# Kernel tuning notes

Measured on AMD Instinct MI355X. Metric: run time of the kernel, lower is better.

Reference implementation:

```python
import jax, jax.numpy as jnp
import numpy as np

NUM_QUBITS = 12
DIM = 2 ** NUM_QUBITS  # 4096
BATCH = 2048
TWO_PI = 2.0 * np.pi


def _diag_phases(p0, p1):
    """Kronecker product of per-qubit diag(exp(i*p0[k]), exp(i*p1[k])) matrices,
    represented as the length-2^n diagonal vector. Phases add under kron of
    diagonal exponentials, so accumulate phases and exponentiate once."""
    ph = jnp.zeros((1,), jnp.float32)
    n = p0.shape[0]
    for k in range(n):  # loop over qubits (small, structural)
        ph = (ph[:, None] + jnp.stack([p0[k], p1[k]])[None, :]).reshape(-1)
    return jnp.exp(1j * ph)  # complex64 diagonal of the 2^n x 2^n operator


def _bs_matrix(n):
    """n-fold Kronecker product of the 50/50 beamsplitter matrix."""
    inv_sqrt2 = np.float32(1.0 / np.sqrt(2.0))
    bs = jnp.array([[1.0, 1j], [1j, 1.0]], dtype=jnp.complex64) * inv_sqrt2
    M = jnp.ones((1, 1), dtype=jnp.complex64)
    for _ in range(n):
        M = jnp.kron(M, bs)
    return M  # [2^n, 2^n]


def setup_inputs() -> dict:
    key = jax.random.key(0)
    k1, k2, k3, k4, k5, k6 = jax.random.split(key, 6)
    return {
        "x_real": jax.random.normal(k1, (BATCH, DIM), dtype=jnp.float32),
        "x_imag": jax.random.normal(k2, (BATCH, DIM), dtype=jnp.float32),
        "alphas": jax.random.uniform(k3, (NUM_QUBITS,), dtype=jnp.float32, maxval=TWO_PI),
        "betas": jax.random.uniform(k4, (NUM_QUBITS,), dtype=jnp.float32, maxval=TWO_PI),
        "thetas": jax.random.uniform(k5, (NUM_QUBITS,), dtype=jnp.float32, maxval=TWO_PI),
        "phis": jax.random.uniform(k6, (NUM_QUBITS,), dtype=jnp.float32, maxval=TWO_PI),
    }


def reference(x_real, x_imag, alphas, betas, thetas, phis):
    x = x_real + 1j * x_imag  # [B, 2^n] complex64
    zeros = jnp.zeros_like(thetas)
    d_in = _diag_phases(alphas, betas)   # input_shifts diagonal
    d_th = _diag_phases(thetas, zeros)   # theta_shifts diagonal
    d_ph = _diag_phases(phis, zeros)     # phi_shifts diagonal
    bs = _bs_matrix(NUM_QUBITS)          # dense tensor-product matrix
    # K.dot(x, M) == x @ M; diagonal matmuls become row-wise elementwise scales.
    out = (x * d_in) @ bs
    out = (out * d_th) @ bs
    out = out * d_ph
    return out
```

## Files before the change

### kernel.cpp

```cpp
#include <hip/hip_runtime.h>
#include <math.h>

#define NQ 12
#define DIM 4096
#define BATCH 2048

typedef float fv4 __attribute__((ext_vector_type(4)));
typedef float fv2 __attribute__((ext_vector_type(2)));

#if defined(__has_builtin)
#if __has_builtin(__builtin_nontemporal_load) && __has_builtin(__builtin_nontemporal_store)
#define NT_LOAD(p)     __builtin_nontemporal_load(p)
#define NT_STORE(p, v) __builtin_nontemporal_store((v), (p))
#endif
#endif
#ifndef NT_LOAD
#define NT_LOAD(p)     (*(p))
#define NT_STORE(p, v) (*(p) = (v))
#endif

__device__ __forceinline__ float2 cmulf(float2 a, float2 b) {
    return make_float2(a.x * b.x - a.y * b.y, a.x * b.y + a.y * b.x);
}

__device__ __forceinline__ void gstage(float (&vr)[16], float (&vi)[16],
                                       float2 m00, float2 m01,
                                       float2 m10, float2 m11, int m) {
#pragma unroll
    for (int r = 0; r < 16; ++r) {
        if (r & m) continue;
        const int p = r | m;
        const float ur = vr[r], ui = vi[r], wr = vr[p], wi = vi[p];
        vr[r] = fmaf(ur, m00.x, fmaf(-ui, m00.y, fmaf(wr, m10.x, -wi * m10.y)));
        vi[r] = fmaf(ur, m00.y, fmaf( ui, m00.x, fmaf(wr, m10.y,  wi * m10.x)));
        vr[p] = fmaf(ur, m01.x, fmaf(-ui, m01.y, fmaf(wr, m11.x, -wi * m11.y)));
        vi[p] = fmaf(ur, m01.y, fmaf( ui, m01.x, fmaf(wr, m11.y,  wi * m11.x)));
    }
}

__device__ __forceinline__ void apply4(float (&vr)[16], float (&vi)[16],
                                       const float2 (*mt)[4],
                                       int q1, int q2, int q4, int q8) {
    float2 a0 = mt[q1][0], a1 = mt[q1][1], a2 = mt[q1][2], a3 = mt[q1][3];
    float2 b0 = mt[q2][0], b1 = mt[q2][1], b2 = mt[q2][2], b3 = mt[q2][3];
    float2 c0 = mt[q4][0], c1 = mt[q4][1], c2 = mt[q4][2], c3 = mt[q4][3];
    float2 d0 = mt[q8][0], d1 = mt[q8][1], d2 = mt[q8][2], d3 = mt[q8][3];
    gstage(vr, vi, a0, a1, a2, a3, 1);
    gstage(vr, vi, b0, b1, b2, b3, 2);
    gstage(vr, vi, c0, c1, c2, c3, 4);
    gstage(vr, vi, d0, d1, d2, d3, 8);
}

template <bool INTERLEAVED>
__global__ __launch_bounds__(256, 4) void qlayer(
        const float* __restrict__ xr, const float* __restrict__ xi,
        const float* __restrict__ alphas, const float* __restrict__ betas,
        const float* __restrict__ thetas, const float* __restrict__ phis,
        float* __restrict__ out) {
    __shared__ float2 lds[DIM];
    __shared__ float2 mt[NQ][4];

    const int t = threadIdx.x;
    const int row = blockIdx.x;
    const int w = t >> 6, l = t & 63;
    const int abase = (w << 10) | (l << 4);

    fv4 lre[4], lim[4];
    {
        const float* xrp = xr + (size_t)row * DIM + abase;
        const float* xip = xi + (size_t)row * DIM + abase;
#pragma unroll
        for (int c = 0; c < 4; ++c) {
            lre[c] = NT_LOAD(reinterpret_cast<const fv4*>(xrp + 4 * c));
            lim[c] = NT_LOAD(reinterpret_cast<const fv4*>(xip + 4 * c));
        }
    }

    if (t < NQ) {
        float sa, ca;
        sincosf(thetas[t], &sa, &ca);
        const float2 h0 = make_float2((ca - 1.f) * 0.5f, sa * 0.5f);
        const float2 h1 = make_float2(-sa * 0.5f, (ca + 1.f) * 0.5f);
        const float al = alphas[t], be = betas[t], ph = phis[t];
        float s, c;
        sincosf(al + ph, &s, &c); mt[t][0] = cmulf(make_float2(c, s), h0);
        sincosf(al, &s, &c);      mt[t][1] = cmulf(make_float2(c, s), h1);
        sincosf(be + ph, &s, &c); mt[t][2] = cmulf(make_float2(c, s), h1);
        sincosf(be, &s, &c);      mt[t][3] = cmulf(make_float2(c, s),
                                                   make_float2(-h0.x, -h0.y));
    }
    __syncthreads();

    float vr[16], vi[16];
#pragma unroll
    for (int c = 0; c < 4; ++c)
#pragma unroll
        for (int j = 0; j < 4; ++j) {
            vr[c * 4 + j] = lre[c][j];
            vi[c * 4 + j] = lim[c][j];
        }

    apply4(vr, vi, mt, 11, 10, 9, 8);

    const int wbase = w << 10;
#pragma unroll
    for (int r = 0; r < 16; ++r) {
        const int s = wbase | (l << 4) | (r ^ (l & 15));
        lds[s] = make_float2(vr[r], vi[r]);
    }
    asm volatile("s_waitcnt lgkmcnt(0)" ::: "memory");
#pragma unroll
    for (int r = 0; r < 16; ++r) {
        const int s = wbase | ((l >> 4) << 8) | (r << 4) | ((l & 15) ^ r);
        const float2 v = lds[s];
        vr[r] = v.x; vi[r] = v.y;
    }

    apply4(vr, vi, mt, 7, 6, 5, 4);

#pragma unroll
    for (int r = 0; r < 16; ++r) {
        const int s = wbase | ((l >> 4) << 8) | (r << 4) | ((l & 15) ^ r);
        lds[s] = make_float2(vr[r], vi[r]);
    }
    __syncthreads();
#pragma unroll
    for (int r = 0; r < 16; ++r) {
        const int s = (r << 8) | (w << 6) | (l & 48) |
                      ((l & 15) ^ ((w << 2) | (l >> 4)));
        const float2 v = lds[s];
        vr[r] = v.x; vi[r] = v.y;
    }

    apply4(vr, vi, mt, 3, 2, 1, 0);

    if (INTERLEAVED) {
        float2* outp = reinterpret_cast<float2*>(out) + (size_t)row * DIM;
#pragma unroll
        for (int r = 0; r < 16; ++r) {
            const int e = (r << 8) | (w << 6) | l;
            fv2 o; o.x = vr[r]; o.y = vi[r];
            NT_STORE(reinterpret_cast<fv2*>(outp + e), o);
        }
    } else {
        float* outp = out + (size_t)row * DIM;
#pragma unroll
        for (int r = 0; r < 16; ++r) {
            const int e = (r << 8) | (w << 6) | l;
            NT_STORE(outp + e, vr[r]);
        }
    }
}

extern "C" void kernel_launch(void* const* d_in, const int* in_sizes, int n_in,
                              void* d_out, int out_size, void* d_ws, size_t ws_size,
                              hipStream_t stream) {
    const float* xr     = (const float*)d_in[0];
    const float* xi     = (const float*)d_in[1];
    const float* alphas = (const float*)d_in[2];
    const float* betas  = (const float*)d_in[3];
    const float* thetas = (const float*)d_in[4];
    const float* phis   = (const float*)d_in[5];

    if (out_size >= 2 * BATCH * DIM) {
        qlayer<true><<<BATCH, 256, 0, stream>>>(xr, xi, alphas, betas, thetas,
                                                phis, (float*)d_out);
    } else {
        qlayer<false><<<BATCH, 256, 0, stream>>>(xr, xi, alphas, betas, thetas,
                                                 phis, (float*)d_out);
    }
}
```

Baseline: 127.9 us.

## Restructure butterfly into four radix-8 stages with 512 threads per row

```diff
diff --git a/kernel.cpp b/kernel.cpp
--- a/kernel.cpp
+++ b/kernel.cpp
@@ -19,15 +19,17 @@
 #define NT_STORE(p, v) (*(p) = (v))
 #endif
 
+__device__ __forceinline__ int swz(int e) { return e ^ ((e >> 4) & 15); }
+
 __device__ __forceinline__ float2 cmulf(float2 a, float2 b) {
     return make_float2(a.x * b.x - a.y * b.y, a.x * b.y + a.y * b.x);
 }
 
-__device__ __forceinline__ void gstage(float (&vr)[16], float (&vi)[16],
-                                       float2 m00, float2 m01,
-                                       float2 m10, float2 m11, int m) {
+__device__ __forceinline__ void applyq(float (&vr)[8], float (&vi)[8],
+                                       const float2 (*mt)[4], int q, int m) {
+    const float2 m00 = mt[q][0], m01 = mt[q][1], m10 = mt[q][2], m11 = mt[q][3];
 #pragma unroll
-    for (int r = 0; r < 16; ++r) {
+    for (int r = 0; r < 8; ++r) {
         if (r & m) continue;
         const int p = r | m;
         const float ur = vr[r], ui = vi[r], wr = vr[p], wi = vi[p];
@@ -38,21 +40,16 @@
     }
 }
 
-__device__ __forceinline__ void apply4(float (&vr)[16], float (&vi)[16],
+__device__ __forceinline__ void apply3(float (&vr)[8], float (&vi)[8],
                                        const float2 (*mt)[4],
-                                       int q1, int q2, int q4, int q8) {
-    float2 a0 = mt[q1][0], a1 = mt[q1][1], a2 = mt[q1][2], a3 = mt[q1][3];
-    float2 b0 = mt[q2][0], b1 = mt[q2][1], b2 = mt[q2][2], b3 = mt[q2][3];
-    float2 c0 = mt[q4][0], c1 = mt[q4][1], c2 = mt[q4][2], c3 = mt[q4][3];
-    float2 d0 = mt[q8][0], d1 = mt[q8][1], d2 = mt[q8][2], d3 = mt[q8][3];
-    gstage(vr, vi, a0, a1, a2, a3, 1);
-    gstage(vr, vi, b0, b1, b2, b3, 2);
-    gstage(vr, vi, c0, c1, c2, c3, 4);
-    gstage(vr, vi, d0, d1, d2, d3, 8);
+                                       int q1, int q2, int q4) {
+    applyq(vr, vi, mt, q1, 1);
+    applyq(vr, vi, mt, q2, 2);
+    applyq(vr, vi, mt, q4, 4);
 }
 
 template <bool INTERLEAVED>
-__global__ __launch_bounds__(256, 4) void qlayer(
+__global__ __launch_bounds__(512, 8) void qlayer(
         const float* __restrict__ xr, const float* __restrict__ xi,
         const float* __restrict__ alphas, const float* __restrict__ betas,
         const float* __restrict__ thetas, const float* __restrict__ phis,
@@ -63,17 +60,15 @@
     const int t = threadIdx.x;
     const int row = blockIdx.x;
     const int w = t >> 6, l = t & 63;
-    const int abase = (w << 10) | (l << 4);
 
-    fv4 lre[4], lim[4];
+    fv4 lre[2], lim[2];
     {
-        const float* xrp = xr + (size_t)row * DIM + abase;
-        const float* xip = xi + (size_t)row * DIM + abase;
-#pragma unroll
-        for (int c = 0; c < 4; ++c) {
-            lre[c] = NT_LOAD(reinterpret_cast<const fv4*>(xrp + 4 * c));
-            lim[c] = NT_LOAD(reinterpret_cast<const fv4*>(xip + 4 * c));
-        }
+        const float* xrp = xr + (size_t)row * DIM + (t << 3);
+        const float* xip = xi + (size_t)row * DIM + (t << 3);
+        lre[0] = NT_LOAD(reinterpret_cast<const fv4*>(xrp));
+        lre[1] = NT_LOAD(reinterpret_cast<const fv4*>(xrp + 4));
+        lim[0] = NT_LOAD(reinterpret_cast<const fv4*>(xip));
+        lim[1] = NT_LOAD(reinterpret_cast<const fv4*>(xip + 4));
     }
 
     if (t < NQ) {
@@ -91,62 +86,65 @@
     }
     __syncthreads();
 
-    float vr[16], vi[16];
+    float vr[8], vi[8];
 #pragma unroll
-    for (int c = 0; c < 4; ++c)
+    for (int j = 0; j < 4; ++j) {
+        vr[j] = lre[0][j];     vi[j] = lim[0][j];
+        vr[4 + j] = lre[1][j]; vi[4 + j] = lim[1][j];
+    }
+
+    apply3(vr, vi, mt, 11, 10, 9);
+
 #pragma unroll
-        for (int j = 0; j < 4; ++j) {
-            vr[c * 4 + j] = lre[c][j];
-            vi[c * 4 + j] = lim[c][j];
-        }
-
-    apply4(vr, vi, mt, 11, 10, 9, 8);
-
-    const int wbase = w << 10;
-#pragma unroll
-    for (int r = 0; r < 16; ++r) {
-        const int s = wbase | (l << 4) | (r ^ (l & 15));
-        lds[s] = make_float2(vr[r], vi[r]);
-    }
+    for (int r = 0; r < 8; ++r)
+        lds[swz((t << 3) | r)] = make_float2(vr[r], vi[r]);
     asm volatile("s_waitcnt lgkmcnt(0)" ::: "memory");
 #pragma unroll
-    for (int r = 0; r < 16; ++r) {
-        const int s = wbase | ((l >> 4) << 8) | (r << 4) | ((l & 15) ^ r);
-        const float2 v = lds[s];
+    for (int r = 0; r < 8; ++r) {
+        const float2 v = lds[swz(((t >> 3) << 6) | (r << 3) | (t & 7))];
         vr[r] = v.x; vi[r] = v.y;
     }
 
-    apply4(vr, vi, mt, 7, 6, 5, 4);
+    apply3(vr, vi, mt, 8, 7, 6);
 
 #pragma unroll
-    for (int r = 0; r < 16; ++r) {
-        const int s = wbase | ((l >> 4) << 8) | (r << 4) | ((l & 15) ^ r);
-        lds[s] = make_float2(vr[r], vi[r]);
-    }
-    __syncthreads();
+    for (int r = 0; r < 8; ++r)
+        lds[swz(((t >> 3) << 6) | (r << 3) | (t & 7))] =
+            make_float2(vr[r], vi[r]);
+    asm volatile("s_waitcnt lgkmcnt(0)" ::: "memory");
 #pragma unroll
-    for (int r = 0; r < 16; ++r) {
-        const int s = (r << 8) | (w << 6) | (l & 48) |
-                      ((l & 15) ^ ((w << 2) | (l >> 4)));
-        const float2 v = lds[s];
+    for (int r = 0; r < 8; ++r) {
+        const float2 v = lds[swz((w << 9) | (r << 6) | l)];
         vr[r] = v.x; vi[r] = v.y;
     }
 
-    apply4(vr, vi, mt, 3, 2, 1, 0);
+    apply3(vr, vi, mt, 5, 4, 3);
+
+#pragma unroll
+    for (int r = 0; r < 8; ++r)
+        lds[swz((w << 9) | (r << 6) | l)] = make_float2(vr[r], vi[r]);
+    __syncthreads();
+#pragma unroll
+    for (int r = 0; r < 8; ++r) {
+        const float2 v = lds[swz((r << 9) | t)];
+        vr[r] = v.x; vi[r] = v.y;
+    }
+
+    apply3(vr, vi, mt, 2, 1, 0);
 
     if (INTERLEAVED) {
         float2* outp = reinterpret_cast<float2*>(out) + (size_t)row * DIM;
 #pragma unroll
-        for (int r = 0; r < 16; ++r) {
-            const int e = (r << 8) | (w << 6) | l;
+        for (int r = 0; r < 8; ++r) {
+            const int e = (r << 9) | t;
             fv2 o; o.x = vr[r]; o.y = vi[r];
             NT_STORE(reinterpret_cast<fv2*>(outp + e), o);
         }
     } else {
         float* outp = out + (size_t)row * DIM;
 #pragma unroll
-        for (int r = 0; r < 16; ++r) {
-            const int e = (r << 8) | (w << 6) | l;
+        for (int r = 0; r < 8; ++r) {
+            const int e = (r << 9) | t;
             NT_STORE(outp + e, vr[r]);
         }
     }
@@ -163,10 +161,10 @@
     const float* phis   = (const float*)d_in[5];
 
     if (out_size >= 2 * BATCH * DIM) {
-        qlayer<true><<<BATCH, 256, 0, stream>>>(xr, xi, alphas, betas, thetas,
+        qlayer<true><<<BATCH, 512, 0, stream>>>(xr, xi, alphas, betas, thetas,
                                                 phis, (float*)d_out);
     } else {
-        qlayer<false><<<BATCH, 256, 0, stream>>>(xr, xi, alphas, betas, thetas,
+        qlayer<false><<<BATCH, 512, 0, stream>>>(xr, xi, alphas, betas, thetas,
                                                  phis, (float*)d_out);
     }
 }
```

Result: faster. 122.1 us (-4.5%).
